# Performance work log

Hardware: AMD Instinct MI355X
Metric: run time of the kernel (lower is better)

## Reference

```python
import jax, jax.numpy as jnp
import numpy as np

N_CELLS = 50000
N_EDGES = 1600000
D_IN = 256
D_OUT = 128
NEG_SLOPE = 0.2


def setup_inputs() -> dict:
    key = jax.random.key(0)
    k1, k2, k3, k4, k5, k6 = jax.random.split(key, 6)
    x = jax.random.normal(k1, (N_CELLS, D_IN), dtype=jnp.float32)
    # xavier_uniform-ish scale for learnable params
    W = jax.random.normal(k2, (D_IN, D_OUT), dtype=jnp.float32) * (1.414 / np.sqrt(D_IN))
    a = jax.random.normal(k3, (2 * D_OUT, 1), dtype=jnp.float32) * (1.414 / np.sqrt(2 * D_OUT))
    n_src = jax.random.randint(k4, (N_EDGES,), 0, N_CELLS, dtype=jnp.int32)
    n_dst = jax.random.randint(k5, (N_EDGES,), 0, N_CELLS, dtype=jnp.int32)
    n_vals = jax.random.uniform(k6, (N_EDGES,), dtype=jnp.float32)
    return {"x": x, "W": W, "a": a, "n_vals": n_vals, "n_src": n_src, "n_dst": n_dst}


def reference(x, W, a, n_vals, n_src, n_dst):
    """HBS forward (m_hop=1, softmax=False, update_func=None).

    out = (N ⊙ A) @ (x @ W), where A_ij = LeakyReLU([m_i || m_j] a) row-normalized
    over the sparsity pattern of N (given as edge list src/dst/vals).
    """
    n_cells = x.shape[0]
    m = x @ W                                  # [n_cells, d_out]
    d_out = m.shape[1]
    # [m_i || m_j] @ a  ==  (m @ a_src)[i] + (m @ a_dst)[j]  -- avoids [E, 2d] concat
    a_src = a[:d_out, 0]
    a_dst = a[d_out:, 0]
    e = jax.nn.leaky_relu(jnp.take(m @ a_src, n_src) + jnp.take(m @ a_dst, n_dst),
                          negative_slope=NEG_SLOPE)   # [E]
    # sparse row normalization (softmax=False branch -> sparse_row_norm)
    row_sum = jax.ops.segment_sum(e, n_src, num_segments=n_cells)  # [n_cells]
    att = e / jnp.take(row_sum, n_src)                              # [E]
    # Hadamard with neighborhood values, then spmm: out_i = sum_j (N*A)_ij m_j
    vals = n_vals * att                                             # [E]
    out = jax.ops.segment_sum(vals[:, None] * m[n_dst], n_src, num_segments=n_cells)
    return out  # update_func=None -> identity
```

## Files before the change

### kernel.cpp

```cpp
#include <hip/hip_runtime.h>

#define D_IN 256
#define D_OUT 128
#define NEG_SLOPE 0.2
#define CAP 128
#define BROW 144

typedef __attribute__((ext_vector_type(8))) short s16x8;
typedef __attribute__((ext_vector_type(4))) float f32x4;

__device__ __forceinline__ unsigned short f2bf(float f) {
    unsigned u = __float_as_uint(f);
    u += 0x7FFFu + ((u >> 16) & 1u);
    return (unsigned short)(u >> 16);
}
__device__ __forceinline__ float bf2f(unsigned short h) {
    return __uint_as_float(((unsigned)h) << 16);
}

__global__ __launch_bounds__(256) void prep_count(
    const float* __restrict__ W, const float* __restrict__ a,
    double* __restrict__ wa,
    unsigned short* __restrict__ wth, unsigned short* __restrict__ wtl,
    const int* __restrict__ src, int* __restrict__ counts4,
    int* __restrict__ rank, int M, int E) {
    if (blockIdx.x == 0) {
        int k = threadIdx.x;
        double s = 0.0, d = 0.0;
        for (int n = 0; n < D_OUT; ++n) {
            double w = (double)W[k * D_OUT + n];
            s += w * (double)a[n];
            d += w * (double)a[D_OUT + n];
        }
        wa[k] = s;
        wa[D_IN + k] = d;
        return;
    }
    if (blockIdx.x <= 128) {
        int idx = (blockIdx.x - 1) * 256 + threadIdx.x;
        int n = idx & 127;
        int k = idx >> 7;
        float w = W[k * D_OUT + n];
        unsigned short h = f2bf(w);
        wth[(size_t)n * D_IN + k] = h;
        wtl[(size_t)n * D_IN + k] = f2bf(w - bf2f(h));
        return;
    }
    int* cnt = counts4 + (size_t)(threadIdx.x & 3) * M;
    int bid  = blockIdx.x - 129;
    int base = (bid * 256 + (int)threadIdx.x) * 4;
    if (base + 4 <= E) {
        int4 s4 = *(const int4*)(src + base);
        int4 r4;
        r4.x = atomicAdd(&cnt[s4.x], 1);
        r4.y = atomicAdd(&cnt[s4.y], 1);
        r4.z = atomicAdd(&cnt[s4.z], 1);
        r4.w = atomicAdd(&cnt[s4.w], 1);
        *(int4*)(rank + base) = r4;
    } else {
        for (int i = base; i < E; ++i) rank[i] = atomicAdd(&cnt[src[i]], 1);
    }
}

__global__ __launch_bounds__(256) void scan1(
    const int* __restrict__ c4, int* __restrict__ bsum, int M) {
    __shared__ int red[256];
    int i = blockIdx.x * 256 + threadIdx.x;
    int tot = 0;
    if (i < M) tot = c4[i] + c4[M + i] + c4[2 * M + i] + c4[3 * M + i];
    red[threadIdx.x] = tot;
    __syncthreads();
    for (int off = 128; off > 0; off >>= 1) {
        if ((int)threadIdx.x < off) red[threadIdx.x] += red[threadIdx.x + off];
        __syncthreads();
    }
    if (threadIdx.x == 0) bsum[blockIdx.x] = red[0];
}

__global__ __launch_bounds__(256) void scan2(
    const int* __restrict__ bsum, int* __restrict__ boff,
    int* __restrict__ rowptr, int NB, int M) {
    __shared__ int part[256];
    int t = threadIdx.x;
    int v = (t < NB) ? bsum[t] : 0;
    part[t] = v;
    __syncthreads();
    for (int off = 1; off < 256; off <<= 1) {
        int u = (t >= off) ? part[t - off] : 0;
        __syncthreads();
        part[t] += u;
        __syncthreads();
    }
    if (t < NB) boff[t] = part[t] - v;
    if (t == NB - 1) rowptr[M] = part[t];
}

__global__ __launch_bounds__(256) void scan3(
    const int* __restrict__ c4, const int* __restrict__ boff,
    int* __restrict__ rowptr, int* __restrict__ base4, int M) {
    __shared__ int part[256];
    int t = threadIdx.x;
    int i = blockIdx.x * 256 + t;
    int c0 = 0, c1 = 0, c2 = 0, c3 = 0;
    if (i < M) {
        c0 = c4[i]; c1 = c4[M + i]; c2 = c4[2 * M + i]; c3 = c4[3 * M + i];
    }
    int tot = c0 + c1 + c2 + c3;
    part[t] = tot;
    __syncthreads();
    for (int off = 1; off < 256; off <<= 1) {
        int u = (t >= off) ? part[t - off] : 0;
        __syncthreads();
        part[t] += u;
        __syncthreads();
    }
    if (i < M) {
        int base = boff[blockIdx.x] + part[t] - tot;
        rowptr[i] = base;
        base4[i]         = base;
        base4[M + i]     = base + c0;
        base4[2 * M + i] = base + c0 + c1;
        base4[3 * M + i] = base + c0 + c1 + c2;
    }
}

__global__ __launch_bounds__(256) void gemm_mfma(
    const float* __restrict__ x,
    const unsigned short* __restrict__ wth, const unsigned short* __restrict__ wtl,
    const double* __restrict__ wa,
    float* __restrict__ m,
    double* __restrict__ svec, double* __restrict__ dvec, int M) {
    __shared__ __align__(16) unsigned char bsm[128 * BROW];

    const int tid  = threadIdx.x;
    const int wave = tid >> 6;
    const int lane = tid & 63;
    const int c    = lane & 15;
    const int q    = lane >> 4;
    const int r0   = blockIdx.x * 64 + wave * 16;
    const int arow  = r0 + c;
    const int arowc = (arow < M) ? arow : (M - 1);

    const int sn = tid >> 1;
    const int sd = tid & 1;
    const unsigned short* sgl = (sd ? wtl : wth) + (size_t)sn * D_IN;
    unsigned char* sls = bsm + sn * BROW + sd * 64;

    f32x4 acc[8];
#pragma unroll
    for (int t = 0; t < 8; ++t) acc[t] = (f32x4){0.f, 0.f, 0.f, 0.f};
    double ps = 0.0, pd = 0.0;

    for (int kt = 0; kt < 8; ++kt) {
        const int kb0 = kt * 32;
        float4 t0 = *(const float4*)(sgl + kb0);
        float4 t1 = *(const float4*)(sgl + kb0 + 8);
        float4 t2 = *(const float4*)(sgl + kb0 + 16);
        float4 t3 = *(const float4*)(sgl + kb0 + 24);
        const int kb = kb0 + q * 8;
        const float* xp = x + (size_t)arowc * D_IN + kb;
        float4 a0 = *(const float4*)(xp);
        float4 a1 = *(const float4*)(xp + 4);
        *(float4*)(sls +  0) = t0;
        *(float4*)(sls + 16) = t1;
        *(float4*)(sls + 32) = t2;
        *(float4*)(sls + 48) = t3;
        __syncthreads();

        float av[8] = {a0.x, a0.y, a0.z, a0.w, a1.x, a1.y, a1.z, a1.w};
#pragma unroll
        for (int j = 0; j < 8; ++j) {
            ps += (double)av[j] * wa[kb + j];
            pd += (double)av[j] * wa[D_IN + kb + j];
        }
        s16x8 ah, al;
#pragma unroll
        for (int j = 0; j < 8; ++j) {
            unsigned short h = f2bf(av[j]);
            ah[j] = (short)h;
            al[j] = (short)f2bf(av[j] - bf2f(h));
        }
#pragma unroll
        for (int t = 0; t < 8; ++t) {
            const unsigned char* bp = bsm + (t * 16 + c) * BROW + q * 16;
            s16x8 bh = *(const s16x8*)(bp);
            s16x8 bl = *(const s16x8*)(bp + 64);
            acc[t] = __builtin_amdgcn_mfma_f32_16x16x32_bf16(al, bh, acc[t], 0, 0, 0);
            acc[t] = __builtin_amdgcn_mfma_f32_16x16x32_bf16(ah, bl, acc[t], 0, 0, 0);
            acc[t] = __builtin_amdgcn_mfma_f32_16x16x32_bf16(ah, bh, acc[t], 0, 0, 0);
        }
        __syncthreads();
    }

    ps += __shfl_xor(ps, 16); ps += __shfl_xor(ps, 32);
    pd += __shfl_xor(pd, 16); pd += __shfl_xor(pd, 32);
    if (q == 0 && arow < M) { svec[arow] = ps; dvec[arow] = pd; }

#pragma unroll
    for (int t = 0; t < 8; ++t) {
#pragma unroll
        for (int reg = 0; reg < 4; ++reg) {
            int r = r0 + q * 4 + reg;
            if (r < M) m[(size_t)r * D_OUT + t * 16 + c] = acc[t][reg];
        }
    }
}

__global__ __launch_bounds__(256) void fill_kernel(
    const int* __restrict__ src, const int* __restrict__ dst,
    const float* __restrict__ nvals, const int* __restrict__ base4,
    const int* __restrict__ rank, int2* __restrict__ edges, int M, int E) {
    const int* bas = base4 + (size_t)(threadIdx.x & 3) * M;
    int base = (blockIdx.x * 256 + (int)threadIdx.x) * 4;
    if (base + 4 <= E) {
        int4   s4 = *(const int4*)(src + base);
        int4   d4 = *(const int4*)(dst + base);
        int4   r4 = *(const int4*)(rank + base);
        float4 n4 = *(const float4*)(nvals + base);
        edges[bas[s4.x] + r4.x] = make_int2(d4.x, __float_as_int(n4.x));
        edges[bas[s4.y] + r4.y] = make_int2(d4.y, __float_as_int(n4.y));
        edges[bas[s4.z] + r4.z] = make_int2(d4.z, __float_as_int(n4.z));
        edges[bas[s4.w] + r4.w] = make_int2(d4.w, __float_as_int(n4.w));
    } else {
        for (int i = base; i < E; ++i)
            edges[bas[src[i]] + rank[i]] = make_int2(dst[i], __float_as_int(nvals[i]));
    }
}

__global__ __launch_bounds__(256) void row_kernel(
    const int* __restrict__ rowptr, const int2* __restrict__ edges,
    const double* __restrict__ svec, const double* __restrict__ dvec,
    const float* __restrict__ m, float* __restrict__ out, int M) {
    __shared__ int   s_dst[4][CAP];
    __shared__ float s_c[4][CAP];
    int w    = threadIdx.x >> 6;
    int lane = threadIdx.x & 63;
    int r    = blockIdx.x * 4 + w;
    if (r >= M) return;
    int beg = rowptr[r], end = rowptr[r + 1], len = end - beg;
    double sr  = svec[r];
    double sum = 0.0;
    for (int j = lane; j < len; j += 64) {
        int2 ed = edges[beg + j];
        double v = sr + dvec[ed.x];
        v = (v > 0.0) ? v : v * NEG_SLOPE;
        sum += v;
        if (j < CAP) {
            s_dst[w][j] = ed.x;
            s_c[w][j]   = (float)((double)__int_as_float(ed.y) * v);
        }
    }
#pragma unroll
    for (int off = 32; off > 0; off >>= 1) sum += __shfl_xor(sum, off);
    float invf = (float)(1.0 / sum);
    __builtin_amdgcn_wave_barrier();

    float2 acc = make_float2(0.f, 0.f);
    int lim = len < CAP ? len : CAP;
    int j = 0;
    for (; j + 16 <= lim; j += 16) {
        float2 mv[16]; float c16[16];
#pragma unroll
        for (int k = 0; k < 16; ++k) {
            int d  = s_dst[w][j + k];
            c16[k] = s_c[w][j + k] * invf;
            mv[k]  = ((const float2*)(m + (size_t)d * D_OUT))[lane];
        }
#pragma unroll
        for (int k = 0; k < 16; ++k) {
            acc.x = fmaf(c16[k], mv[k].x, acc.x);
            acc.y = fmaf(c16[k], mv[k].y, acc.y);
        }
    }
    for (; j < lim; ++j) {
        int d = s_dst[w][j];
        float cc = s_c[w][j] * invf;
        float2 mv = ((const float2*)(m + (size_t)d * D_OUT))[lane];
        acc.x = fmaf(cc, mv.x, acc.x);
        acc.y = fmaf(cc, mv.y, acc.y);
    }
    for (; j < len; ++j) {
        int2 ed = edges[beg + j];
        double v = sr + dvec[ed.x];
        v = (v > 0.0) ? v : v * NEG_SLOPE;
        float cc = (float)((double)__int_as_float(ed.y) * v) * invf;
        float2 mv = ((const float2*)(m + (size_t)ed.x * D_OUT))[lane];
        acc.x = fmaf(cc, mv.x, acc.x);
        acc.y = fmaf(cc, mv.y, acc.y);
    }
    ((float2*)(out + (size_t)r * D_OUT))[lane] = acc;
}

extern "C" void kernel_launch(void* const* d_in, const int* in_sizes, int n_in,
                              void* d_out, int out_size, void* d_ws, size_t ws_size,
                              hipStream_t stream) {
    const float* x     = (const float*)d_in[0];
    const float* W     = (const float*)d_in[1];
    const float* a     = (const float*)d_in[2];
    const float* nvals = (const float*)d_in[3];
    const int*   nsrc  = (const int*)d_in[4];
    const int*   ndst  = (const int*)d_in[5];
    const int M = in_sizes[0] / D_IN;
    const int E = in_sizes[4];
    float* out = (float*)d_out;

    char* ws = (char*)d_ws;
    size_t off = 0;
    float*  m    = (float*)(ws + off);           off += (size_t)M * D_OUT * sizeof(float);
    unsigned short* wth = (unsigned short*)(ws + off); off += (size_t)D_OUT * D_IN * 2;
    unsigned short* wtl = (unsigned short*)(ws + off); off += (size_t)D_OUT * D_IN * 2;
    double* wa   = (double*)(ws + off);          off += (size_t)2 * D_IN * sizeof(double);
    double* svec = (double*)(ws + off);          off += (size_t)M * sizeof(double);
    double* dvec = (double*)(ws + off);          off += (size_t)M * sizeof(double);
    int*    counts4 = (int*)(ws + off); off += ((size_t)4 * M * sizeof(int) + 15) & ~15ull;
    int*    base4   = (int*)(ws + off); off += ((size_t)4 * M * sizeof(int) + 15) & ~15ull;
    int*    rowptr  = (int*)(ws + off); off += ((size_t)(M + 1) * sizeof(int) + 15) & ~15ull;
    int*    bsum    = (int*)(ws + off); off += (256 * sizeof(int) + 15) & ~15ull;
    int*    boff    = (int*)(ws + off); off += (256 * sizeof(int) + 15) & ~15ull;
    int*    rank    = (int*)(ws + off); off += (size_t)E * sizeof(int);
    int2*   edges   = (int2*)(ws + off); off += (size_t)E * sizeof(int2);

    hipMemsetAsync(counts4, 0, (size_t)4 * M * sizeof(int), stream);

    const int countBlocks = (E + 1023) / 1024;
    const int gemmBlocks  = (M + 63) / 64;
    const int NB          = (M + 255) / 256;

    prep_count<<<129 + countBlocks, 256, 0, stream>>>(W, a, wa, wth, wtl, nsrc, counts4, rank, M, E);
    scan1<<<NB, 256, 0, stream>>>(counts4, bsum, M);
    scan2<<<1, 256, 0, stream>>>(bsum, boff, rowptr, NB, M);
    scan3<<<NB, 256, 0, stream>>>(counts4, boff, rowptr, base4, M);
    gemm_mfma<<<gemmBlocks, 256, 0, stream>>>(x, wth, wtl, wa, m, svec, dvec, M);
    fill_kernel<<<countBlocks, 256, 0, stream>>>(nsrc, ndst, nvals, base4, rank, edges, M, E);
    row_kernel<<<(M + 3) / 4, 256, 0, stream>>>(rowptr, edges, svec, dvec, m, out, M);
}
```

Baseline: 363.6 us.

## Split prep/count kernels and gather rows with float4 half-wave edge pairs

The row aggregation kernel now splits each wave into two half-waves that each process alternate edges, loading 16-byte float4 chunks of the gathered m rows instead of 8-byte float2. The halves are combined with a cross-lane shuffle at the end, and odd edge counts are padded with a zero sentinel entry. The goal is wider memory transactions and more edges in flight per wave, at the cost of an extra reduction. The fused prep/count kernel is also split into two separate launches, which adds one launch.

New measurement: 364.9 us. Within noise of the previous version (+0.4%).

```diff
diff --git a/kernel.cpp b/kernel.cpp
--- a/kernel.cpp
+++ b/kernel.cpp
@@ -18,12 +18,10 @@
     return __uint_as_float(((unsigned)h) << 16);
 }
 
-__global__ __launch_bounds__(256) void prep_count(
+__global__ __launch_bounds__(256) void prep_w(
     const float* __restrict__ W, const float* __restrict__ a,
     double* __restrict__ wa,
-    unsigned short* __restrict__ wth, unsigned short* __restrict__ wtl,
-    const int* __restrict__ src, int* __restrict__ counts4,
-    int* __restrict__ rank, int M, int E) {
+    unsigned short* __restrict__ wth, unsigned short* __restrict__ wtl) {
     if (blockIdx.x == 0) {
         int k = threadIdx.x;
         double s = 0.0, d = 0.0;
@@ -36,19 +34,20 @@
         wa[D_IN + k] = d;
         return;
     }
-    if (blockIdx.x <= 128) {
-        int idx = (blockIdx.x - 1) * 256 + threadIdx.x;
-        int n = idx & 127;
-        int k = idx >> 7;
-        float w = W[k * D_OUT + n];
-        unsigned short h = f2bf(w);
-        wth[(size_t)n * D_IN + k] = h;
-        wtl[(size_t)n * D_IN + k] = f2bf(w - bf2f(h));
-        return;
-    }
+    int idx = (blockIdx.x - 1) * 256 + threadIdx.x;
+    int n = idx & 127;
+    int k = idx >> 7;
+    float w = W[k * D_OUT + n];
+    unsigned short h = f2bf(w);
+    wth[(size_t)n * D_IN + k] = h;
+    wtl[(size_t)n * D_IN + k] = f2bf(w - bf2f(h));
+}
+
+__global__ __launch_bounds__(256) void count_rank(
+    const int* __restrict__ src, int* __restrict__ counts4,
+    int* __restrict__ rank, int M, int E) {
     int* cnt = counts4 + (size_t)(threadIdx.x & 3) * M;
-    int bid  = blockIdx.x - 129;
-    int base = (bid * 256 + (int)threadIdx.x) * 4;
+    int base = (blockIdx.x * 256 + (int)threadIdx.x) * 4;
     if (base + 4 <= E) {
         int4 s4 = *(const int4*)(src + base);
         int4 r4;
@@ -250,45 +249,66 @@
             s_c[w][j]   = (float)((double)__int_as_float(ed.y) * v);
         }
     }
+    if (lane == 0 && len < CAP) { s_dst[w][len] = 0; s_c[w][len] = 0.f; }
 #pragma unroll
     for (int off = 32; off > 0; off >>= 1) sum += __shfl_xor(sum, off);
     float invf = (float)(1.0 / sum);
     __builtin_amdgcn_wave_barrier();
 
-    float2 acc = make_float2(0.f, 0.f);
-    int lim = len < CAP ? len : CAP;
+    const int h  = lane >> 5;
+    const int l5 = lane & 31;
+    float4 acc = make_float4(0.f, 0.f, 0.f, 0.f);
+    int lim  = len < CAP ? len : CAP;
+    int limp = (lim + 1) & ~1;
     int j = 0;
-    for (; j + 16 <= lim; j += 16) {
-        float2 mv[16]; float c16[16];
-#pragma unroll
-        for (int k = 0; k < 16; ++k) {
-            int d  = s_dst[w][j + k];
-            c16[k] = s_c[w][j + k] * invf;
-            mv[k]  = ((const float2*)(m + (size_t)d * D_OUT))[lane];
-        }
-#pragma unroll
-        for (int k = 0; k < 16; ++k) {
-            acc.x = fmaf(c16[k], mv[k].x, acc.x);
-            acc.y = fmaf(c16[k], mv[k].y, acc.y);
-        }
-    }
-    for (; j < lim; ++j) {
-        int d = s_dst[w][j];
-        float cc = s_c[w][j] * invf;
-        float2 mv = ((const float2*)(m + (size_t)d * D_OUT))[lane];
+    for (; j + 16 <= limp; j += 16) {
+        float4 mv[8]; float c8[8];
+#pragma unroll
+        for (int k = 0; k < 8; ++k) {
+            int e = j + 2 * k + h;
+            int d = s_dst[w][e];
+            c8[k] = s_c[w][e] * invf;
+            mv[k] = *(const float4*)(m + (size_t)d * D_OUT + l5 * 4);
+        }
+#pragma unroll
+        for (int k = 0; k < 8; ++k) {
+            acc.x = fmaf(c8[k], mv[k].x, acc.x);
+            acc.y = fmaf(c8[k], mv[k].y, acc.y);
+            acc.z = fmaf(c8[k], mv[k].z, acc.z);
+            acc.w = fmaf(c8[k], mv[k].w, acc.w);
+        }
+    }
+    for (; j < limp; j += 2) {
+        int e = j + h;
+        int d = s_dst[w][e];
+        float cc = s_c[w][e] * invf;
+        float4 mv = *(const float4*)(m + (size_t)d * D_OUT + l5 * 4);
         acc.x = fmaf(cc, mv.x, acc.x);
         acc.y = fmaf(cc, mv.y, acc.y);
-    }
-    for (; j < len; ++j) {
-        int2 ed = edges[beg + j];
-        double v = sr + dvec[ed.x];
-        v = (v > 0.0) ? v : v * NEG_SLOPE;
-        float cc = (float)((double)__int_as_float(ed.y) * v) * invf;
-        float2 mv = ((const float2*)(m + (size_t)ed.x * D_OUT))[lane];
+        acc.z = fmaf(cc, mv.z, acc.z);
+        acc.w = fmaf(cc, mv.w, acc.w);
+    }
+    for (; j < len; j += 2) {
+        int e = j + h;
+        int d = 0; float cc = 0.f;
+        if (e < len) {
+            int2 ed = edges[beg + e];
+            double v = sr + dvec[ed.x];
+            v = (v > 0.0) ? v : v * NEG_SLOPE;
+            cc = (float)((double)__int_as_float(ed.y) * v) * invf;
+            d  = ed.x;
+        }
+        float4 mv = *(const float4*)(m + (size_t)d * D_OUT + l5 * 4);
         acc.x = fmaf(cc, mv.x, acc.x);
         acc.y = fmaf(cc, mv.y, acc.y);
-    }
-    ((float2*)(out + (size_t)r * D_OUT))[lane] = acc;
+        acc.z = fmaf(cc, mv.z, acc.z);
+        acc.w = fmaf(cc, mv.w, acc.w);
+    }
+    acc.x += __shfl_xor(acc.x, 32);
+    acc.y += __shfl_xor(acc.y, 32);
+    acc.z += __shfl_xor(acc.z, 32);
+    acc.w += __shfl_xor(acc.w, 32);
+    if (h == 0) *(float4*)(out + (size_t)r * D_OUT + l5 * 4) = acc;
 }
 
 extern "C" void kernel_launch(void* const* d_in, const int* in_sizes, int n_in,
@@ -326,7 +346,8 @@
     const int gemmBlocks  = (M + 63) / 64;
     const int NB          = (M + 255) / 256;
 
-    prep_count<<<129 + countBlocks, 256, 0, stream>>>(W, a, wa, wth, wtl, nsrc, counts4, rank, M, E);
+    prep_w<<<129, 256, 0, stream>>>(W, a, wa, wth, wtl);
+    count_rank<<<countBlocks, 256, 0, stream>>>(nsrc, counts4, rank, M, E);
     scan1<<<NB, 256, 0, stream>>>(counts4, bsum, M);
     scan2<<<1, 256, 0, stream>>>(bsum, boff, rowptr, NB, M);
     scan3<<<NB, 256, 0, stream>>>(counts4, boff, rowptr, base4, M);
```
